# Optimization experiments

Hardware: AMD Instinct MI355X
Metric: run time of the kernel (lower is better)

Reference implementation:

```python
import jax, jax.numpy as jnp
import numpy as np

DIM = 1536      # model dim
NH = 12         # num heads
HD = 128        # head dim
F, H, W = 3, 26, 48   # video latent grid (frames, height, width)
S = F * H * W   # sequence length = 3744
B = 1
EPS = 1e-6
C2 = HD // 2    # 64 rotary pairs per head
SPLITS = [C2 - 2 * (C2 // 3), C2 // 3, C2 // 3]  # [22, 21, 21] for (f, h, w)


def _rope_angles():
    """Wan rope_params: concat of per-axis inverse-frequency angle tables, [1024, 64]."""
    def rp(dim):  # returns [1024, dim//2]
        inv = 1.0 / (10000.0 ** (np.arange(0, dim, 2, dtype=np.float64) / dim))
        return np.outer(np.arange(1024, dtype=np.float64), inv)
    a = np.concatenate([rp(HD - 4 * (HD // 6)), rp(2 * (HD // 6)), rp(2 * (HD // 6))], axis=1)
    return jnp.asarray(a, jnp.float32)


def setup_inputs() -> dict:
    key = jax.random.key(0)
    ks = jax.random.split(key, 9)
    std = DIM ** -0.5
    return {
        "x": jax.random.normal(ks[0], (B, S, DIM), jnp.float32),
        "wq": jax.random.normal(ks[1], (DIM, DIM), jnp.float32) * std,
        "bq": jnp.zeros((DIM,), jnp.float32),
        "wk": jax.random.normal(ks[2], (DIM, DIM), jnp.float32) * std,
        "bk": jnp.zeros((DIM,), jnp.float32),
        "wv": jax.random.normal(ks[3], (DIM, DIM), jnp.float32) * std,
        "bv": jnp.zeros((DIM,), jnp.float32),
        "wo": jax.random.normal(ks[4], (DIM, DIM), jnp.float32) * std,
        "bo": jnp.zeros((DIM,), jnp.float32),
        "gq": jnp.ones((DIM,), jnp.float32),   # WanRMSNorm weight for q
        "gk": jnp.ones((DIM,), jnp.float32),   # WanRMSNorm weight for k
        "freqs": _rope_angles(),                # [1024, 64] rotary angles
        "seq_lens": jnp.full((B,), S, jnp.int32),
    }


def _rmsnorm(y, g):
    return y * jax.lax.rsqrt(jnp.mean(jnp.square(y), axis=-1, keepdims=True) + EPS) * g


def _rope_grid(freqs):
    """Build per-position rotary angles [S, C2] from the 3D grid (F,H,W)."""
    af = freqs[:F, :SPLITS[0]]                       # [F, 22]
    ah = freqs[:H, SPLITS[0]:SPLITS[0] + SPLITS[1]]  # [H, 21]
    aw = freqs[:W, SPLITS[0] + SPLITS[1]:]           # [W, 21]
    ang = jnp.concatenate([
        jnp.broadcast_to(af[:, None, None, :], (F, H, W, SPLITS[0])),
        jnp.broadcast_to(ah[None, :, None, :], (F, H, W, SPLITS[1])),
        jnp.broadcast_to(aw[None, None, :, :], (F, H, W, SPLITS[2])),
    ], axis=-1)
    return ang.reshape(S, C2)


def _rope_apply(t, cos, sin):
    # t: [B, S, NH, HD]; pairs (even, odd) rotated by angle.
    tp = t.reshape(B, S, NH, C2, 2)
    xr, xi = tp[..., 0], tp[..., 1]
    yr = xr * cos - xi * sin
    yi = xr * sin + xi * cos
    return jnp.stack([yr, yi], axis=-1).reshape(B, S, NH, HD)


def reference(x, wq, bq, wk, bk, wv, bv, wo, bo, gq, gk, freqs, seq_lens):
    q = _rmsnorm(x @ wq.T + bq, gq).reshape(B, S, NH, HD)
    k = _rmsnorm(x @ wk.T + bk, gk).reshape(B, S, NH, HD)
    v = (x @ wv.T + bv).reshape(B, S, NH, HD)

    ang = _rope_grid(freqs)                    # [S, C2]
    cos = jnp.cos(ang)[None, :, None, :]       # [1, S, 1, C2]
    sin = jnp.sin(ang)[None, :, None, :]
    q = _rope_apply(q, cos, sin)
    k = _rope_apply(k, cos, sin)

    scale = HD ** -0.5
    scores = jnp.einsum('bqhd,bkhd->bhqk', q, k) * scale   # [B, NH, S, S]
    kmask = jnp.arange(S)[None, :] < seq_lens[:, None]     # [B, S]
    scores = jnp.where(kmask[:, None, None, :], scores, jnp.float32(-1e9))
    attn = jax.nn.softmax(scores, axis=-1)
    out = jnp.einsum('bhqk,bkhd->bqhd', attn, v).reshape(B, S, DIM)
    return out @ wo.T + bo
```

## Files before the change

kernel.cpp:

```cpp
#include <hip/hip_runtime.h>
#include <stdint.h>


#define DIM   1536
#define S_TOT 3744
#define NHEAD 12
#define HD    128
#define QT2   30
#define KVT   59
#define KSPLIT 2

using short8 = __attribute__((ext_vector_type(8))) short;
using f32x4  = __attribute__((ext_vector_type(4))) float;
using f32x16 = __attribute__((ext_vector_type(16))) float;
using f32x2  = __attribute__((ext_vector_type(2))) float;

__device__ __forceinline__ unsigned short f2bf(float f) {
  unsigned u = __builtin_bit_cast(unsigned, f);
  u += 0x7fffu + ((u >> 16) & 1u);
  return (unsigned short)(u >> 16);
}

__device__ __forceinline__ short8 mk8(unsigned a, unsigned b, unsigned c, unsigned d) {
  union { unsigned u[4]; short8 s; } x;
  x.u[0] = a; x.u[1] = b; x.u[2] = c; x.u[3] = d;
  return x.s;
}

__device__ __forceinline__ void gl_lds16(const void* g, void* l) {
  auto gp = (const __attribute__((address_space(1))) unsigned int*)g;
  auto lp = (__attribute__((address_space(3))) unsigned int*)(uintptr_t)l;
  __builtin_amdgcn_global_load_lds(gp, lp, 16, 0, 0);
}

#define NX4 (S_TOT * DIM / 4)
#define NW4 (DIM * DIM / 4)
__global__ __launch_bounds__(256) void cvt5_kernel(
    const float* __restrict__ x, const float* __restrict__ wq,
    const float* __restrict__ wk, const float* __restrict__ wv,
    const float* __restrict__ wo,
    unsigned short* __restrict__ xb, unsigned short* __restrict__ wqb,
    unsigned short* __restrict__ wkb, unsigned short* __restrict__ wvb,
    unsigned short* __restrict__ wob) {
  int gid = blockIdx.x * 256 + threadIdx.x;
  const float* src; unsigned short* dst; int off;
  if (gid < NX4)                { src = x;  dst = xb;  off = gid; }
  else if (gid < NX4 + NW4)     { src = wq; dst = wqb; off = gid - NX4; }
  else if (gid < NX4 + 2 * NW4) { src = wk; dst = wkb; off = gid - NX4 - NW4; }
  else if (gid < NX4 + 3 * NW4) { src = wv; dst = wvb; off = gid - NX4 - 2 * NW4; }
  else if (gid < NX4 + 4 * NW4) { src = wo; dst = wob; off = gid - NX4 - 3 * NW4; }
  else return;
  float4 v = ((const float4*)src)[off];
  ushort4 o;
  o.x = f2bf(v.x); o.y = f2bf(v.y); o.z = f2bf(v.z); o.w = f2bf(v.w);
  ((ushort4*)dst)[off] = o;
}

__device__ __forceinline__ void gemm_body(const unsigned short* __restrict__ A,
                                          const unsigned short* __restrict__ W,
                                          const float* __restrict__ bias,
                                          float* __restrict__ outF,
                                          unsigned short* __restrict__ outB,
                                          int M, int mode, int m0, int n0) {
  constexpr int K = DIM, N = DIM;
  __shared__ unsigned short As[2][128 * 32];
  __shared__ unsigned short Ws[2][128 * 32];
  int tid = threadIdx.x;
  int w = tid >> 6, lane = tid & 63;
  int wr = w >> 1, wc = w & 1, q4 = lane >> 4, ql = lane & 15;

  f32x4 acc[4][4];
  const f32x4 zero4 = {0.f, 0.f, 0.f, 0.f};
#pragma unroll
  for (int i = 0; i < 4; i++)
#pragma unroll
    for (int j = 0; j < 4; j++) acc[i][j] = zero4;

  for (int k0 = 0; k0 < K; k0 += 64) {
    __syncthreads();
#pragma unroll
    for (int half = 0; half < 2; half++) {
#pragma unroll
      for (int r = 0; r < 2; r++) {
        int idx = r * 256 + tid;
        int row = idx >> 2, ch = idx & 3;
        int am = m0 + row; am = (am < M) ? am : (M - 1);
        gl_lds16(A + (size_t)am * K + k0 + half * 32 + ch * 8, &As[half][idx * 8]);
        gl_lds16(W + (size_t)(n0 + row) * K + k0 + half * 32 + ch * 8, &Ws[half][idx * 8]);
      }
    }
    __syncthreads();
#pragma unroll
    for (int half = 0; half < 2; half++) {
      short8 af[4], wf[4];
#pragma unroll
      for (int i = 0; i < 4; i++)
        af[i] = *(const short8*)&As[half][(wr * 64 + i * 16 + ql) * 32 + q4 * 8];
#pragma unroll
      for (int j = 0; j < 4; j++)
        wf[j] = *(const short8*)&Ws[half][(wc * 64 + j * 16 + ql) * 32 + q4 * 8];
#pragma unroll
      for (int i = 0; i < 4; i++)
#pragma unroll
        for (int j = 0; j < 4; j++)
          acc[i][j] = __builtin_amdgcn_mfma_f32_16x16x32_bf16(af[i], wf[j], acc[i][j], 0, 0, 0);
    }
  }

  float bb[4];
#pragma unroll
  for (int j = 0; j < 4; j++) bb[j] = bias[n0 + wc * 64 + j * 16 + ql];
#pragma unroll
  for (int i = 0; i < 4; i++) {
#pragma unroll
    for (int rg = 0; rg < 4; rg++) {
      int row = m0 + wr * 64 + i * 16 + q4 * 4 + rg;
      if (row < M) {
#pragma unroll
        for (int j = 0; j < 4; j++) {
          int col = n0 + wc * 64 + j * 16 + ql;
          float v = acc[i][j][rg] + bb[j];
          if (mode == 0) outF[(size_t)row * N + col] = v;
          else           outB[(size_t)row * N + col] = f2bf(v);
        }
      }
    }
  }
}

__global__ __launch_bounds__(256, 4) void gemm_qkv_kernel(
    const unsigned short* __restrict__ xb,
    const unsigned short* __restrict__ wqb, const unsigned short* __restrict__ wkb,
    const unsigned short* __restrict__ wvb,
    const float* __restrict__ bq, const float* __restrict__ bk, const float* __restrict__ bv,
    float* __restrict__ Yq, float* __restrict__ Yk, unsigned short* __restrict__ Vb) {
  const int NWG = 3 * 30 * 12;
  int bid = blockIdx.x;
  int xcd = bid & 7, bix = bid >> 3;
  int wg = xcd * (NWG >> 3) + bix;
  int z = wg / 360;
  int r = wg - z * 360;
  int m = r / 12, n = r % 12;
  const unsigned short* W = (z == 0) ? wqb : ((z == 1) ? wkb : wvb);
  const float* bias       = (z == 0) ? bq  : ((z == 1) ? bk  : bv);
  float* outF             = (z == 0) ? Yq  : Yk;
  gemm_body(xb, W, bias, outF, Vb, S_TOT, (z == 2) ? 1 : 0, m * 128, n * 128);
}

__global__ __launch_bounds__(256, 4) void gemm_out_kernel(
    const unsigned short* __restrict__ AO, const unsigned short* __restrict__ wob,
    const float* __restrict__ bo, float* __restrict__ out) {
  const int NWG = 30 * 12;
  int bid = blockIdx.x;
  int xcd = bid & 7, bix = bid >> 3;
  int wg = xcd * (NWG >> 3) + bix;
  int m = wg / 12, n = wg % 12;
  gemm_body(AO, wob, bo, out, nullptr, S_TOT, 0, m * 128, n * 128);
}

__global__ __launch_bounds__(256) void normrope_kernel(
    const float* __restrict__ Yq, const float* __restrict__ Yk,
    const float* __restrict__ gq, const float* __restrict__ gk,
    const float* __restrict__ freqs,
    unsigned short* __restrict__ Qb, unsigned short* __restrict__ Kb) {
  int s = blockIdx.x;
  int tid = threadIdx.x;
  int w = tid >> 6, lane = tid & 63;
  const f32x2* yq2 = (const f32x2*)(Yq + (size_t)s * DIM);
  const f32x2* yk2 = (const f32x2*)(Yk + (size_t)s * DIM);
  f32x2 vq[3], vk[3];
  float ssq = 0.f, ssk = 0.f;
#pragma unroll
  for (int r = 0; r < 3; r++) {
    int p = tid + 256 * r;
    vq[r] = yq2[p]; vk[r] = yk2[p];
    ssq += vq[r].x * vq[r].x + vq[r].y * vq[r].y;
    ssk += vk[r].x * vk[r].x + vk[r].y * vk[r].y;
  }
#pragma unroll
  for (int d = 1; d < 64; d <<= 1) {
    ssq += __shfl_xor(ssq, d);
    ssk += __shfl_xor(ssk, d);
  }
  __shared__ float rq[4], rk[4];
  if (lane == 0) { rq[w] = ssq; rk[w] = ssk; }
  __syncthreads();
  float tq = rq[0] + rq[1] + rq[2] + rq[3];
  float tk = rk[0] + rk[1] + rk[2] + rk[3];
  const float SM_L2 = 0.08838834764831845f * 1.4426950408889634f;
  float invq = rsqrtf(tq * (1.f / DIM) + 1e-6f) * SM_L2;
  float invk = rsqrtf(tk * (1.f / DIM) + 1e-6f);

  int fi = s / (26 * 48);
  int hi = (s / 48) % 26;
  int wi = s % 48;
#pragma unroll
  for (int r = 0; r < 3; r++) {
    int p = tid + 256 * r;
    int c = p & 63;
    int frow = (c < 22) ? fi : ((c < 43) ? hi : wi);
    float ang = freqs[frow * 64 + c];
    float sn, cs;
    __sincosf(ang, &sn, &cs);
    {
      float a = vq[r].x * invq * gq[2 * p];
      float b = vq[r].y * invq * gq[2 * p + 1];
      ushort2 o; o.x = f2bf(a * cs - b * sn); o.y = f2bf(a * sn + b * cs);
      ((ushort2*)Qb)[(size_t)s * (DIM / 2) + p] = o;
    }
    {
      float a = vk[r].x * invk * gk[2 * p];
      float b = vk[r].y * invk * gk[2 * p + 1];
      ushort2 o; o.x = f2bf(a * cs - b * sn); o.y = f2bf(a * sn + b * cs);
      ((ushort2*)Kb)[(size_t)s * (DIM / 2) + p] = o;
    }
  }
}

__global__ __launch_bounds__(256) void vtrans_kernel(const unsigned short* __restrict__ Vb,
                                                     unsigned short* __restrict__ Vt) {
  int d0 = blockIdx.x * 64, s0 = blockIdx.y * 64;
  __shared__ unsigned short t[64][65];
  int tid = threadIdx.x;
#pragma unroll
  for (int r = 0; r < 4; r++) {
    int idx = r * 256 + tid;
    int sr = idx >> 4, c4 = (idx & 15) * 4;
    ushort4 v; v.x = v.y = v.z = v.w = 0;
    int s = s0 + sr;
    if (s < S_TOT) v = *(const ushort4*)(Vb + (size_t)s * DIM + d0 + c4);
    t[sr][c4 + 0] = v.x; t[sr][c4 + 1] = v.y; t[sr][c4 + 2] = v.z; t[sr][c4 + 3] = v.w;
  }
  __syncthreads();
#pragma unroll
  for (int r = 0; r < 4; r++) {
    int idx = r * 256 + tid;
    int dr = idx >> 4, s4 = (idx & 15) * 4;
    if (s0 + s4 < S_TOT) {
      ushort4 v;
      v.x = t[s4 + 0][dr]; v.y = t[s4 + 1][dr]; v.z = t[s4 + 2][dr]; v.w = t[s4 + 3][dr];
      *(ushort4*)(Vt + (size_t)(d0 + dr) * S_TOT + s0 + s4) = v;
    }
  }
}

__global__ __launch_bounds__(256, 2) void attn_kernel(
    const unsigned short* __restrict__ Qb, const unsigned short* __restrict__ Kb,
    const unsigned short* __restrict__ Vt,
    float* __restrict__ Opart, float2* __restrict__ Ml,
    const int* __restrict__ seq_lens) {
  const int NWG = QT2 * NHEAD * KSPLIT;
  int bid = blockIdx.x;
  int xcd = bid & 7, bix = bid >> 3;
  const int qc = NWG >> 3;
  int wg = xcd * qc + bix;
  int qt  = wg % QT2;
  int rem = wg / QT2;
  int h    = rem >> 1;
  int sidx = rem & 1;
  int tbeg = sidx ? 30 : 0;
  int tend = sidx ? KVT : 30;

  int tid = threadIdx.x;
  int wv = tid >> 6, lane = tid & 63;
  int lo = lane & 31, hf = lane >> 5;
  int seqlen = seq_lens[0]; if (seqlen > S_TOT) seqlen = S_TOT;

  __shared__ unsigned short Kl[2][64 * 128];
  __shared__ unsigned short Vl[2][128 * 64];

  int q0 = qt * 128 + wv * 32;
  bool wact = (q0 < S_TOT);
  const size_t hoff = (size_t)h * HD;

  auto stage = [&](int buf, int t) {
    int k0 = t * 64;
    const unsigned short* kseg = Kb + (size_t)k0 * DIM + hoff;
#pragma unroll
    for (int r = 0; r < 4; r++) {
      int idx = r * 256 + tid;
      int row = idx >> 4, c = idx & 15;
      int g = c ^ (row & 15);
      gl_lds16(kseg + (size_t)row * DIM + g * 8, &Kl[buf][idx * 8]);
    }
    int kmax = S_TOT - 8 - k0;
#pragma unroll
    for (int r = 0; r < 4; r++) {
      int idx = r * 256 + tid;
      int row = idx >> 3, c = idx & 7;
      int g = c ^ (row & 7);
      int kc = g * 8; if (kc > kmax) kc = kmax;
      gl_lds16(Vt + (hoff + row) * S_TOT + k0 + kc, &Vl[buf][idx * 8]);
    }
  };

  short8 qf[8];
  {
    int qrow = q0 + lo; if (qrow > S_TOT - 1) qrow = S_TOT - 1;
#pragma unroll
    for (int ks = 0; ks < 8; ks++)
      qf[ks] = *(const short8*)(Qb + (size_t)qrow * DIM + hoff + ks * 16 + hf * 8);
  }
  asm volatile("s_waitcnt vmcnt(0)" ::: "memory");

  f32x16 o[4];
#pragma unroll
  for (int dq = 0; dq < 4; dq++)
#pragma unroll
    for (int r = 0; r < 16; r++) o[dq][r] = 0.f;
  float m_run = -3.0e38f, l_run = 0.f;

  stage(0, tbeg);

  for (int t = tbeg; t < tend; ++t) {
    int cur = (t - tbeg) & 1;
    int k0 = t * 64;
    __builtin_amdgcn_s_barrier();
    asm volatile("" ::: "memory");
    if (t + 1 < tend) {
      stage(cur ^ 1, t + 1);
      asm volatile("s_waitcnt vmcnt(8)" ::: "memory");
    } else {
      asm volatile("s_waitcnt vmcnt(0)" ::: "memory");
    }
    __builtin_amdgcn_sched_barrier(0);
    __builtin_amdgcn_s_barrier();
    asm volatile("" ::: "memory");
    if (!wact) continue;

    f32x16 s0, s1;
#pragma unroll
    for (int r = 0; r < 16; r++) { s0[r] = 0.f; s1[r] = 0.f; }
    __builtin_amdgcn_s_setprio(1);
#pragma unroll
    for (int ks = 0; ks < 8; ks++) {
      int sl = ((ks * 2 + hf) ^ (lo & 15)) * 8;
      short8 kf0 = *(const short8*)&Kl[cur][lo * 128 + sl];
      short8 kf1 = *(const short8*)&Kl[cur][(32 + lo) * 128 + sl];
      s0 = __builtin_amdgcn_mfma_f32_32x32x16_bf16(kf0, qf[ks], s0, 0, 0, 0);
      s1 = __builtin_amdgcn_mfma_f32_32x32x16_bf16(kf1, qf[ks], s1, 0, 0, 0);
    }
    __builtin_amdgcn_s_setprio(0);

    if (k0 + 64 > seqlen) {
#pragma unroll
      for (int r = 0; r < 16; r++) {
        int key0 = k0 + (r & 3) + 8 * (r >> 2) + 4 * hf;
        if (key0      >= seqlen) s0[r] = -3.0e38f;
        if (key0 + 32 >= seqlen) s1[r] = -3.0e38f;
      }
    }

    float mloc = s0[0];
#pragma unroll
    for (int r = 1; r < 16; r++) mloc = fmaxf(mloc, s0[r]);
#pragma unroll
    for (int r = 0; r < 16; r++) mloc = fmaxf(mloc, s1[r]);
    mloc = fmaxf(mloc, __shfl_xor(mloc, 32));

    if (!__all(mloc <= m_run + 8.0f)) {
      float mnew = fmaxf(m_run, mloc);
      float alpha = exp2f(m_run - mnew);
      m_run = mnew;
      l_run *= alpha;
      int lb = lane & 32;
      float ar[16];
#pragma unroll
      for (int r = 0; r < 16; r++)
        ar[r] = __shfl(alpha, ((r & 3) + 8 * (r >> 2) + 4 * hf) | lb);
#pragma unroll
      for (int dq = 0; dq < 4; dq++)
#pragma unroll
        for (int r = 0; r < 16; r++) o[dq][r] *= ar[r];
    }

    float lloc = 0.f;
    short8 pa[4];
    {
      float p[16];
#pragma unroll
      for (int r = 0; r < 16; r++) { p[r] = exp2f(s0[r] - m_run); lloc += p[r]; }
      unsigned pr[8];
#pragma unroll
      for (int i = 0; i < 8; i++)
        asm("v_cvt_pk_bf16_f32 %0, %1, %2" : "=v"(pr[i]) : "v"(p[2 * i]), "v"(p[2 * i + 1]));
      asm volatile("v_permlane32_swap_b32 %0, %1" : "+v"(pr[0]), "+v"(pr[2]));
      asm volatile("v_permlane32_swap_b32 %0, %1" : "+v"(pr[1]), "+v"(pr[3]));
      asm volatile("v_permlane32_swap_b32 %0, %1" : "+v"(pr[4]), "+v"(pr[6]));
      asm volatile("v_permlane32_swap_b32 %0, %1" : "+v"(pr[5]), "+v"(pr[7]));
      pa[0] = mk8(pr[0], pr[1], pr[2], pr[3]);
      pa[1] = mk8(pr[4], pr[5], pr[6], pr[7]);
    }
    {
      float p[16];
#pragma unroll
      for (int r = 0; r < 16; r++) { p[r] = exp2f(s1[r] - m_run); lloc += p[r]; }
      unsigned pr[8];
#pragma unroll
      for (int i = 0; i < 8; i++)
        asm("v_cvt_pk_bf16_f32 %0, %1, %2" : "=v"(pr[i]) : "v"(p[2 * i]), "v"(p[2 * i + 1]));
      asm volatile("v_permlane32_swap_b32 %0, %1" : "+v"(pr[0]), "+v"(pr[2]));
      asm volatile("v_permlane32_swap_b32 %0, %1" : "+v"(pr[1]), "+v"(pr[3]));
      asm volatile("v_permlane32_swap_b32 %0, %1" : "+v"(pr[4]), "+v"(pr[6]));
      asm volatile("v_permlane32_swap_b32 %0, %1" : "+v"(pr[5]), "+v"(pr[7]));
      pa[2] = mk8(pr[0], pr[1], pr[2], pr[3]);
      pa[3] = mk8(pr[4], pr[5], pr[6], pr[7]);
    }
    lloc += __shfl_xor(lloc, 32);
    l_run += lloc;

    __builtin_amdgcn_s_setprio(1);
#pragma unroll
    for (int kh2 = 0; kh2 < 4; kh2++) {
      int sl = ((kh2 * 2 + hf) ^ (lo & 7)) * 8;
#pragma unroll
      for (int dq = 0; dq < 4; dq++) {
        short8 vb = *(const short8*)&Vl[cur][(dq * 32 + lo) * 64 + sl];
        o[dq] = __builtin_amdgcn_mfma_f32_32x32x16_bf16(pa[kh2], vb, o[dq], 0, 0, 0);
      }
    }
    __builtin_amdgcn_s_setprio(0);
  }

  if (wact) {
    size_t ob = (((size_t)sidx * NHEAD + h) * QT2 + qt) * (128 * 128);
#pragma unroll
    for (int dq = 0; dq < 4; dq++)
#pragma unroll
      for (int r = 0; r < 16; r++) {
        int row = wv * 32 + (r & 3) + 8 * (r >> 2) + 4 * hf;
        Opart[ob + (size_t)row * 128 + dq * 32 + lo] = o[dq][r];
      }
    if (lane < 32) {
      float2 ml; ml.x = m_run; ml.y = l_run;
      Ml[((size_t)(sidx * NHEAD + h) * QT2 + qt) * 128 + wv * 32 + lo] = ml;
    }
  }
}

__global__ __launch_bounds__(256) void reduce_kernel(
    const float* __restrict__ Opart, const float2* __restrict__ Ml,
    unsigned short* __restrict__ AO) {
  int flat = blockIdx.x * 256 + threadIdx.x;
  int d = flat & 127;
  int r = flat >> 7;
  int h = r / S_TOT;
  int q = r - h * S_TOT;
  int qt = q >> 7, qi = q & 127;
  size_t ob = (((size_t)h * QT2) + qt) * (128 * 128) + (size_t)qi * 128 + d;
  const size_t so = (size_t)NHEAD * QT2 * 128 * 128;
  int mb = (h * QT2 + qt) * 128 + qi;
  const int sm = NHEAD * QT2 * 128;
  float2 ml0 = Ml[mb], ml1 = Ml[mb + sm];
  float mm = fmaxf(ml0.x, ml1.x);
  float w0 = exp2f(ml0.x - mm), w1 = exp2f(ml1.x - mm);
  float l = w0 * ml0.y + w1 * ml1.y;
  float v = (w0 * Opart[ob] + w1 * Opart[ob + so]) / l;
  AO[(size_t)q * DIM + h * HD + d] = f2bf(v);
}

extern "C" void kernel_launch(void* const* d_in, const int* in_sizes, int n_in,
                              void* d_out, int out_size, void* d_ws, size_t ws_size,
                              hipStream_t stream) {
  const float* x    = (const float*)d_in[0];
  const float* wq   = (const float*)d_in[1];
  const float* bq   = (const float*)d_in[2];
  const float* wk   = (const float*)d_in[3];
  const float* bk   = (const float*)d_in[4];
  const float* wv   = (const float*)d_in[5];
  const float* bv   = (const float*)d_in[6];
  const float* wo   = (const float*)d_in[7];
  const float* bo   = (const float*)d_in[8];
  const float* gq   = (const float*)d_in[9];
  const float* gk   = (const float*)d_in[10];
  const float* freqs = (const float*)d_in[11];
  const int*   seq  = (const int*)d_in[12];

  char* ws = (char*)d_ws;
  const size_t SZ_X = (size_t)S_TOT * DIM * 2;
  const size_t SZ_W = (size_t)DIM * DIM * 2;
  const size_t SZ_Y = (size_t)S_TOT * DIM * 4;

  size_t off = 0;
  unsigned short* xb  = (unsigned short*)(ws + off); off += SZ_X;
  unsigned short* wob = (unsigned short*)(ws + off); off += SZ_W;
  float*          Yq  = (float*)(ws + off);          off += SZ_Y;
  float*          Yk  = (float*)(ws + off);          off += SZ_Y;
  unsigned short* wqb = (unsigned short*)(ws + off); off += SZ_W;
  unsigned short* wkb = (unsigned short*)(ws + off); off += SZ_W;
  unsigned short* wvb = (unsigned short*)(ws + off); off += SZ_W;
  unsigned short* Vb  = (unsigned short*)(ws + off); off += SZ_X;
  unsigned short* Qb  = (unsigned short*)(ws + off); off += SZ_X;
  unsigned short* Kb  = (unsigned short*)(ws + off); off += SZ_X;
  unsigned short* Vt  = (unsigned short*)(ws + off); off += SZ_X;
  unsigned short* AO  = (unsigned short*)(ws + off); off += SZ_X;

  float*  Opart = (float*)Yq;
  float2* Ml    = (float2*)((char*)Yq +
                  (size_t)KSPLIT * NHEAD * QT2 * 128 * 128 * sizeof(float));

  int total4 = NX4 + 4 * NW4;
  cvt5_kernel<<<dim3((total4 + 255) / 256), 256, 0, stream>>>(
      x, wq, wk, wv, wo, xb, wqb, wkb, wvb, wob);

  gemm_qkv_kernel<<<dim3(3 * 30 * 12), 256, 0, stream>>>(
      xb, wqb, wkb, wvb, bq, bk, bv, Yq, Yk, Vb);

  normrope_kernel<<<dim3(S_TOT), 256, 0, stream>>>(Yq, Yk, gq, gk, freqs, Qb, Kb);

  vtrans_kernel<<<dim3(DIM / 64, (S_TOT + 63) / 64), 256, 0, stream>>>(Vb, Vt);

  attn_kernel<<<dim3(QT2 * NHEAD * KSPLIT), 256, 0, stream>>>(
      Qb, Kb, Vt, Opart, Ml, seq);

  reduce_kernel<<<dim3(NHEAD * S_TOT * HD / 256), 256, 0, stream>>>(Opart, Ml, AO);

  gemm_out_kernel<<<dim3(30 * 12), 256, 0, stream>>>(AO, wob, bo, (float*)d_out);
}
```

Baseline: 401.1 us.

## Drop attention split-K and reduce kernel; emit bf16 Q/K projections

Removes the two-way KV split in attention so each workgroup processes all KV tiles and writes normalized bf16 output directly, eliminating the partial-output buffers and the separate reduce kernel. The QKV GEMM now stores Q and K pre-norm results as bf16 instead of fp32, halving that intermediate traffic into the norm/rope kernel. This trades attention grid parallelism (half as many workgroups) for less memory traffic and one fewer launch, and slightly reduces precision before RMSNorm.

```diff
diff --git a/kernel.cpp b/kernel.cpp
--- a/kernel.cpp
+++ b/kernel.cpp
@@ -8,7 +8,6 @@
 #define HD    128
 #define QT2   30
 #define KVT   59
-#define KSPLIT 2
 
 using short8 = __attribute__((ext_vector_type(8))) short;
 using f32x4  = __attribute__((ext_vector_type(4))) float;
@@ -19,6 +18,10 @@
   unsigned u = __builtin_bit_cast(unsigned, f);
   u += 0x7fffu + ((u >> 16) & 1u);
   return (unsigned short)(u >> 16);
+}
+
+__device__ __forceinline__ float bf2f(unsigned short u) {
+  return __builtin_bit_cast(float, (unsigned)u << 16);
 }
 
 __device__ __forceinline__ short8 mk8(unsigned a, unsigned b, unsigned c, unsigned d) {
@@ -133,7 +136,8 @@
     const unsigned short* __restrict__ wqb, const unsigned short* __restrict__ wkb,
     const unsigned short* __restrict__ wvb,
     const float* __restrict__ bq, const float* __restrict__ bk, const float* __restrict__ bv,
-    float* __restrict__ Yq, float* __restrict__ Yk, unsigned short* __restrict__ Vb) {
+    unsigned short* __restrict__ Yqb, unsigned short* __restrict__ Ykb,
+    unsigned short* __restrict__ Vb) {
   const int NWG = 3 * 30 * 12;
   int bid = blockIdx.x;
   int xcd = bid & 7, bix = bid >> 3;
@@ -143,8 +147,8 @@
   int m = r / 12, n = r % 12;
   const unsigned short* W = (z == 0) ? wqb : ((z == 1) ? wkb : wvb);
   const float* bias       = (z == 0) ? bq  : ((z == 1) ? bk  : bv);
-  float* outF             = (z == 0) ? Yq  : Yk;
-  gemm_body(xb, W, bias, outF, Vb, S_TOT, (z == 2) ? 1 : 0, m * 128, n * 128);
+  unsigned short* dst     = (z == 0) ? Yqb : ((z == 1) ? Ykb : Vb);
+  gemm_body(xb, W, bias, nullptr, dst, S_TOT, 1, m * 128, n * 128);
 }
 
 __global__ __launch_bounds__(256, 4) void gemm_out_kernel(
@@ -159,21 +163,23 @@
 }
 
 __global__ __launch_bounds__(256) void normrope_kernel(
-    const float* __restrict__ Yq, const float* __restrict__ Yk,
+    const unsigned short* __restrict__ Yqb, const unsigned short* __restrict__ Ykb,
     const float* __restrict__ gq, const float* __restrict__ gk,
     const float* __restrict__ freqs,
     unsigned short* __restrict__ Qb, unsigned short* __restrict__ Kb) {
   int s = blockIdx.x;
   int tid = threadIdx.x;
   int w = tid >> 6, lane = tid & 63;
-  const f32x2* yq2 = (const f32x2*)(Yq + (size_t)s * DIM);
-  const f32x2* yk2 = (const f32x2*)(Yk + (size_t)s * DIM);
+  const ushort2* yq2 = (const ushort2*)(Yqb + (size_t)s * DIM);
+  const ushort2* yk2 = (const ushort2*)(Ykb + (size_t)s * DIM);
   f32x2 vq[3], vk[3];
   float ssq = 0.f, ssk = 0.f;
 #pragma unroll
   for (int r = 0; r < 3; r++) {
     int p = tid + 256 * r;
-    vq[r] = yq2[p]; vk[r] = yk2[p];
+    ushort2 uq = yq2[p], uk = yk2[p];
+    vq[r].x = bf2f(uq.x); vq[r].y = bf2f(uq.y);
+    vk[r].x = bf2f(uk.x); vk[r].y = bf2f(uk.y);
     ssq += vq[r].x * vq[r].x + vq[r].y * vq[r].y;
     ssk += vk[r].x * vk[r].x + vk[r].y * vk[r].y;
   }
@@ -246,20 +252,14 @@
 
 __global__ __launch_bounds__(256, 2) void attn_kernel(
     const unsigned short* __restrict__ Qb, const unsigned short* __restrict__ Kb,
-    const unsigned short* __restrict__ Vt,
-    float* __restrict__ Opart, float2* __restrict__ Ml,
+    const unsigned short* __restrict__ Vt, unsigned short* __restrict__ AO,
     const int* __restrict__ seq_lens) {
-  const int NWG = QT2 * NHEAD * KSPLIT;
+  const int NWG = QT2 * NHEAD;
   int bid = blockIdx.x;
   int xcd = bid & 7, bix = bid >> 3;
-  const int qc = NWG >> 3;
-  int wg = xcd * qc + bix;
-  int qt  = wg % QT2;
-  int rem = wg / QT2;
-  int h    = rem >> 1;
-  int sidx = rem & 1;
-  int tbeg = sidx ? 30 : 0;
-  int tend = sidx ? KVT : 30;
+  int wg = xcd * (NWG >> 3) + bix;
+  int qt = wg % QT2;
+  int h  = wg / QT2;
 
   int tid = threadIdx.x;
   int wv = tid >> 6, lane = tid & 63;
@@ -310,14 +310,14 @@
     for (int r = 0; r < 16; r++) o[dq][r] = 0.f;
   float m_run = -3.0e38f, l_run = 0.f;
 
-  stage(0, tbeg);
-
-  for (int t = tbeg; t < tend; ++t) {
-    int cur = (t - tbeg) & 1;
+  stage(0, 0);
+
+  for (int t = 0; t < KVT; ++t) {
+    int cur = t & 1;
     int k0 = t * 64;
     __builtin_amdgcn_s_barrier();
     asm volatile("" ::: "memory");
-    if (t + 1 < tend) {
+    if (t + 1 < KVT) {
       stage(cur ^ 1, t + 1);
       asm volatile("s_waitcnt vmcnt(8)" ::: "memory");
     } else {
@@ -423,40 +423,20 @@
   }
 
   if (wact) {
-    size_t ob = (((size_t)sidx * NHEAD + h) * QT2 + qt) * (128 * 128);
+    float il = 1.0f / l_run;
+    int lb = lane & 32;
+    float ilr[16];
+#pragma unroll
+    for (int r = 0; r < 16; r++)
+      ilr[r] = __shfl(il, ((r & 3) + 8 * (r >> 2) + 4 * hf) | lb);
 #pragma unroll
     for (int dq = 0; dq < 4; dq++)
 #pragma unroll
       for (int r = 0; r < 16; r++) {
-        int row = wv * 32 + (r & 3) + 8 * (r >> 2) + 4 * hf;
-        Opart[ob + (size_t)row * 128 + dq * 32 + lo] = o[dq][r];
+        int row = q0 + (r & 3) + 8 * (r >> 2) + 4 * hf;
+        AO[(size_t)row * DIM + hoff + dq * 32 + lo] = f2bf(o[dq][r] * ilr[r]);
       }
-    if (lane < 32) {
-      float2 ml; ml.x = m_run; ml.y = l_run;
-      Ml[((size_t)(sidx * NHEAD + h) * QT2 + qt) * 128 + wv * 32 + lo] = ml;
-    }
-  }
-}
-
-__global__ __launch_bounds__(256) void reduce_kernel(
-    const float* __restrict__ Opart, const float2* __restrict__ Ml,
-    unsigned short* __restrict__ AO) {
-  int flat = blockIdx.x * 256 + threadIdx.x;
-  int d = flat & 127;
-  int r = flat >> 7;
-  int h = r / S_TOT;
-  int q = r - h * S_TOT;
-  int qt = q >> 7, qi = q & 127;
-  size_t ob = (((size_t)h * QT2) + qt) * (128 * 128) + (size_t)qi * 128 + d;
-  const size_t so = (size_t)NHEAD * QT2 * 128 * 128;
-  int mb = (h * QT2 + qt) * 128 + qi;
-  const int sm = NHEAD * QT2 * 128;
-  float2 ml0 = Ml[mb], ml1 = Ml[mb + sm];
-  float mm = fmaxf(ml0.x, ml1.x);
-  float w0 = exp2f(ml0.x - mm), w1 = exp2f(ml1.x - mm);
-  float l = w0 * ml0.y + w1 * ml1.y;
-  float v = (w0 * Opart[ob] + w1 * Opart[ob + so]) / l;
-  AO[(size_t)q * DIM + h * HD + d] = f2bf(v);
+  }
 }
 
 extern "C" void kernel_launch(void* const* d_in, const int* in_sizes, int n_in,
@@ -479,13 +459,12 @@
   char* ws = (char*)d_ws;
   const size_t SZ_X = (size_t)S_TOT * DIM * 2;
   const size_t SZ_W = (size_t)DIM * DIM * 2;
-  const size_t SZ_Y = (size_t)S_TOT * DIM * 4;
 
   size_t off = 0;
   unsigned short* xb  = (unsigned short*)(ws + off); off += SZ_X;
   unsigned short* wob = (unsigned short*)(ws + off); off += SZ_W;
-  float*          Yq  = (float*)(ws + off);          off += SZ_Y;
-  float*          Yk  = (float*)(ws + off);          off += SZ_Y;
+  unsigned short* Yqb = (unsigned short*)(ws + off); off += SZ_X;
+  unsigned short* Ykb = (unsigned short*)(ws + off); off += SZ_X;
   unsigned short* wqb = (unsigned short*)(ws + off); off += SZ_W;
   unsigned short* wkb = (unsigned short*)(ws + off); off += SZ_W;
   unsigned short* wvb = (unsigned short*)(ws + off); off += SZ_W;
@@ -495,25 +474,18 @@
   unsigned short* Vt  = (unsigned short*)(ws + off); off += SZ_X;
   unsigned short* AO  = (unsigned short*)(ws + off); off += SZ_X;
 
-  float*  Opart = (float*)Yq;
-  float2* Ml    = (float2*)((char*)Yq +
-                  (size_t)KSPLIT * NHEAD * QT2 * 128 * 128 * sizeof(float));
-
   int total4 = NX4 + 4 * NW4;
   cvt5_kernel<<<dim3((total4 + 255) / 256), 256, 0, stream>>>(
       x, wq, wk, wv, wo, xb, wqb, wkb, wvb, wob);
 
   gemm_qkv_kernel<<<dim3(3 * 30 * 12), 256, 0, stream>>>(
-      xb, wqb, wkb, wvb, bq, bk, bv, Yq, Yk, Vb);
-
-  normrope_kernel<<<dim3(S_TOT), 256, 0, stream>>>(Yq, Yk, gq, gk, freqs, Qb, Kb);
+      xb, wqb, wkb, wvb, bq, bk, bv, Yqb, Ykb, Vb);
+
+  normrope_kernel<<<dim3(S_TOT), 256, 0, stream>>>(Yqb, Ykb, gq, gk, freqs, Qb, Kb);
 
   vtrans_kernel<<<dim3(DIM / 64, (S_TOT + 63) / 64), 256, 0, stream>>>(Vb, Vt);
 
-  attn_kernel<<<dim3(QT2 * NHEAD * KSPLIT), 256, 0, stream>>>(
-      Qb, Kb, Vt, Opart, Ml, seq);
-
-  reduce_kernel<<<dim3(NHEAD * S_TOT * HD / 256), 256, 0, stream>>>(Opart, Ml, AO);
+  attn_kernel<<<dim3(QT2 * NHEAD), 256, 0, stream>>>(Qb, Kb, Vt, AO, seq);
 
   gemm_out_kernel<<<dim3(30 * 12), 256, 0, stream>>>(AO, wob, bo, (float*)d_out);
 }
```

Result: no change. 402.6 us (+0.4%).
